# Kernel optimization log

Measured on AMD Instinct MI355X. Metric: run time of the kernel, lower is better.

Reference implementation:

```python
import jax, jax.numpy as jnp
import numpy as np


def setup_inputs() -> dict:
    key = jax.random.key(0)
    k1, k2 = jax.random.split(key)
    B, N, M, D = 4, 8192, 8192, 3
    input1 = jax.random.normal(k1, (B, N, D), dtype=jnp.float32)
    input2 = jax.random.normal(k2, (B, M, D), dtype=jnp.float32)
    return {"input1": input1, "input2": input2}


def reference(input1, input2):
    x2 = jnp.sum(input1 * input1, axis=-1)              # [B, N]
    y2 = jnp.sum(input2 * input2, axis=-1)              # [B, M]
    xy = jnp.einsum('bnd,bmd->bnm', input1, input2)     # [B, N, M]
    d2 = x2[:, :, None] + y2[:, None, :] - 2.0 * xy     # [B, N, M]
    d2 = jnp.maximum(d2, 0.0)
    dist1 = jnp.min(d2, axis=2)  # [B, N] nearest in input2 for each point in input1
    dist2 = jnp.min(d2, axis=1)  # [B, M] nearest in input1 for each point in input2
    # Chamfer loss: mean of both directional terms
    return jnp.mean(dist1) + jnp.mean(dist2)
```

## Files before the change

kernel.cpp:

```cpp
#include <hip/hip_runtime.h>

#define NB    4
#define NPTS  8192
#define QPB   64
#define WPB   8

typedef float v2f __attribute__((ext_vector_type(2)));

struct TPair { v2f xx, yy, zz, ww; };

__global__ void pack_pts(const float* __restrict__ a, const float* __restrict__ b,
                         float4* __restrict__ q4a, float4* __restrict__ q4b,
                         TPair* __restrict__ tpa, TPair* __restrict__ tpb) {
    const int npair = NB * NPTS / 2;
    int i = blockIdx.x * blockDim.x + threadIdx.x;
    const float* src = a;
    float4* q4 = q4a;  TPair* tp = tpa;
    int p = i;
    if (i >= npair) { src = b; q4 = q4b; tp = tpb; p = i - npair; }

    float x0 = src[6*p+0], y0 = src[6*p+1], z0 = src[6*p+2];
    float x1 = src[6*p+3], y1 = src[6*p+4], z1 = src[6*p+5];
    float w0 = 0.5f * (x0*x0 + y0*y0 + z0*z0);
    float w1 = 0.5f * (x1*x1 + y1*y1 + z1*z1);
    q4[2*p]   = make_float4(x0, y0, z0, w0);
    q4[2*p+1] = make_float4(x1, y1, z1, w1);
    TPair t;
    t.xx = (v2f){x0, x1}; t.yy = (v2f){y0, y1};
    t.zz = (v2f){z0, z1}; t.ww = (v2f){w0, w1};
    tp[p] = t;
}

#define GROUP(XX, YY, ZZ, WW, ACC) do {                                        \
    v2f r_;                                                                    \
    asm("v_pk_mul_f32 %0, %1, %2"     : "=v"(r_) : "v"(nqx), "s"(XX));         \
    asm("v_pk_fma_f32 %0, %1, %2, %0" : "+v"(r_) : "v"(nqy), "s"(YY));         \
    asm("v_pk_fma_f32 %0, %1, %2, %0" : "+v"(r_) : "v"(nqz), "s"(ZZ));         \
    asm("v_pk_add_f32 %0, %0, %1"     : "+v"(r_) : "s"(WW));                   \
    asm("v_min3_f32 %0, %0, %1, %2"   : "+v"(ACC) : "v"(r_.x), "v"(r_.y));     \
} while (0)

__launch_bounds__(512, 8)
__global__ void chamfer_min(const float4* __restrict__ q4a, const float4* __restrict__ q4b,
                            const TPair* __restrict__ tpa, const TPair* __restrict__ tpb,
                            float* __restrict__ accum) {
    __shared__ float red[512];

    const int dir = blockIdx.y;
    const int bb  = blockIdx.x / (NPTS / QPB);
    const int blk = blockIdx.x % (NPTS / QPB);

    const float4* __restrict__ Q = (dir == 0 ? q4a : q4b) + bb * NPTS;
    const TPair*  __restrict__ T = (dir == 0 ? tpb : tpa) + bb * (NPTS / 2);

    const int lane = threadIdx.x & 63;
    const int wave = __builtin_amdgcn_readfirstlane((int)(threadIdx.x >> 6));

    const float4 q = Q[blk * QPB + lane];
    v2f nqx = (v2f){-q.x, -q.x};
    v2f nqy = (v2f){-q.y, -q.y};
    v2f nqz = (v2f){-q.z, -q.z};

    const int PPW = NPTS / 2 / WPB;
    const TPair* __restrict__ Tw = T + wave * PPW;

    float acc0 = 1e30f, acc1 = 1e30f, acc2 = 1e30f, acc3 = 1e30f;

    for (int p = 0; p < PPW; p += 4) {
        TPair t0 = Tw[p + 0];
        TPair t1 = Tw[p + 1];
        TPair t2 = Tw[p + 2];
        TPair t3 = Tw[p + 3];
        GROUP(t0.xx, t0.yy, t0.zz, t0.ww, acc0);
        GROUP(t1.xx, t1.yy, t1.zz, t1.ww, acc1);
        GROUP(t2.xx, t2.yy, t2.zz, t2.ww, acc2);
        GROUP(t3.xx, t3.yy, t3.zz, t3.ww, acc3);
    }
    float acc = fminf(fminf(acc0, acc1), fminf(acc2, acc3));

    red[threadIdx.x] = acc;
    __syncthreads();

    if (threadIdx.x < 64) {
        float v = red[lane];
#pragma unroll
        for (int w = 1; w < WPB; ++w) v = fminf(v, red[lane + 64 * w]);
        float dist = fmaxf(2.0f * (q.w + v), 0.0f);
        for (int off = 32; off > 0; off >>= 1)
            dist += __shfl_xor(dist, off, 64);
        if (lane == 0) atomicAdd(&accum[dir], dist);
    }
}

__global__ void finish(const float* __restrict__ accum, float* __restrict__ out) {
    out[0] = (accum[0] + accum[1]) * (1.0f / (NB * NPTS));
}

extern "C" void kernel_launch(void* const* d_in, const int* in_sizes, int n_in,
                              void* d_out, int out_size, void* d_ws, size_t ws_size,
                              hipStream_t stream) {
    const float* in1 = (const float*)d_in[0];
    const float* in2 = (const float*)d_in[1];

    const int tot   = NB * NPTS;
    const int npair = tot / 2;

    char* ws = (char*)d_ws;
    float*  accum = (float*)ws;
    float4* q4a   = (float4*)(ws + 256);
    float4* q4b   = q4a + tot;
    TPair*  tpa   = (TPair*)(q4b + tot);
    TPair*  tpb   = tpa + npair;

    hipMemsetAsync(accum, 0, 2 * sizeof(float), stream);

    pack_pts<<<dim3((2 * npair) / 256), 256, 0, stream>>>(in1, in2, q4a, q4b, tpa, tpb);

    dim3 grid(NB * (NPTS / QPB), 2);
    chamfer_min<<<grid, 512, 0, stream>>>(q4a, q4b, tpa, tpb, accum);

    finish<<<1, 1, 0, stream>>>(accum, (float*)d_out);
}
```

Before: 72.88 us.

## Swap roles: hold queries in registers, stream targets per lane

The min kernel is inverted. Before, each lane held one query and targets were broadcast through scalar operands. Now each block keeps 16 queries uniformly in registers as pre-negated packed pairs and each lane streams its own target pairs with vector loads, software-prefetched one iteration ahead. Each loaded target pair is reused across 16 queries, and the per-query minimum is reduced with wave shuffles and a small shared array. The cost is higher register pressure (launch bounds lowered to 3 waves per SIMD), more blocks, and a larger packed query buffer.

New measurement: 81.48 us. 11.8% more time.

```diff
diff --git a/kernel.cpp b/kernel.cpp
--- a/kernel.cpp
+++ b/kernel.cpp
@@ -2,93 +2,121 @@
 
 #define NB    4
 #define NPTS  8192
-#define QPB   64
-#define WPB   8
+#define QPB2  16
+#define TPB   256
+#define ITERS (NPTS / 2 / TPB)
 
 typedef float v2f __attribute__((ext_vector_type(2)));
+typedef float v4f __attribute__((ext_vector_type(4)));
 
 struct TPair { v2f xx, yy, zz, ww; };
 
 __global__ void pack_pts(const float* __restrict__ a, const float* __restrict__ b,
-                         float4* __restrict__ q4a, float4* __restrict__ q4b,
-                         TPair* __restrict__ tpa, TPair* __restrict__ tpb) {
+                         TPair* __restrict__ tpa, TPair* __restrict__ tpb,
+                         float* __restrict__ nqa, float* __restrict__ nqb) {
     const int npair = NB * NPTS / 2;
     int i = blockIdx.x * blockDim.x + threadIdx.x;
-    const float* src = a;
-    float4* q4 = q4a;  TPair* tp = tpa;
+    const float* src = a;  TPair* tp = tpa;  float* nq = nqa;
     int p = i;
-    if (i >= npair) { src = b; q4 = q4b; tp = tpb; p = i - npair; }
+    if (i >= npair) { src = b; tp = tpb; nq = nqb; p = i - npair; }
 
     float x0 = src[6*p+0], y0 = src[6*p+1], z0 = src[6*p+2];
     float x1 = src[6*p+3], y1 = src[6*p+4], z1 = src[6*p+5];
     float w0 = 0.5f * (x0*x0 + y0*y0 + z0*z0);
     float w1 = 0.5f * (x1*x1 + y1*y1 + z1*z1);
-    q4[2*p]   = make_float4(x0, y0, z0, w0);
-    q4[2*p+1] = make_float4(x1, y1, z1, w1);
+
     TPair t;
     t.xx = (v2f){x0, x1}; t.yy = (v2f){y0, y1};
     t.zz = (v2f){z0, z1}; t.ww = (v2f){w0, w1};
     tp[p] = t;
+
+    v4f* o = (v4f*)(nq + (size_t)2 * p * 8);
+    o[0] = (v4f){-x0, -x0, -y0, -y0};
+    o[1] = (v4f){-z0, -z0,  w0, 0.f};
+    o[2] = (v4f){-x1, -x1, -y1, -y1};
+    o[3] = (v4f){-z1, -z1,  w1, 0.f};
 }
 
-#define GROUP(XX, YY, ZZ, WW, ACC) do {                                        \
-    v2f r_;                                                                    \
-    asm("v_pk_mul_f32 %0, %1, %2"     : "=v"(r_) : "v"(nqx), "s"(XX));         \
-    asm("v_pk_fma_f32 %0, %1, %2, %0" : "+v"(r_) : "v"(nqy), "s"(YY));         \
-    asm("v_pk_fma_f32 %0, %1, %2, %0" : "+v"(r_) : "v"(nqz), "s"(ZZ));         \
-    asm("v_pk_add_f32 %0, %0, %1"     : "+v"(r_) : "s"(WW));                   \
-    asm("v_min3_f32 %0, %0, %1, %2"   : "+v"(ACC) : "v"(r_.x), "v"(r_.y));     \
+#define GROUPV(J) do {                                                          \
+    v2f r_;                                                                     \
+    asm("v_pk_mul_f32 %0, %1, %2"     : "=v"(r_) : "v"(qn[3*(J)+0]), "v"(xx_)); \
+    asm("v_pk_fma_f32 %0, %1, %2, %0" : "+v"(r_) : "v"(qn[3*(J)+1]), "v"(yy_)); \
+    asm("v_pk_fma_f32 %0, %1, %2, %0" : "+v"(r_) : "v"(qn[3*(J)+2]), "v"(zz_)); \
+    asm("v_pk_add_f32 %0, %0, %1"     : "+v"(r_) : "v"(ww_));                   \
+    asm("v_min3_f32 %0, %0, %1, %2"   : "+v"(acc[J]) : "v"(r_.x), "v"(r_.y));   \
 } while (0)
 
-__launch_bounds__(512, 8)
-__global__ void chamfer_min(const float4* __restrict__ q4a, const float4* __restrict__ q4b,
-                            const TPair* __restrict__ tpa, const TPair* __restrict__ tpb,
+__launch_bounds__(TPB, 3)
+__global__ void chamfer_min(const TPair* __restrict__ tpa, const TPair* __restrict__ tpb,
+                            const float* __restrict__ nqa, const float* __restrict__ nqb,
                             float* __restrict__ accum) {
-    __shared__ float red[512];
+    __shared__ float red[4][QPB2];
 
-    const int dir = blockIdx.y;
-    const int bb  = blockIdx.x / (NPTS / QPB);
-    const int blk = blockIdx.x % (NPTS / QPB);
+    const int qblk = blockIdx.x;
+    const int bb   = blockIdx.y;
+    const int dir  = blockIdx.z;
 
-    const float4* __restrict__ Q = (dir == 0 ? q4a : q4b) + bb * NPTS;
-    const TPair*  __restrict__ T = (dir == 0 ? tpb : tpa) + bb * (NPTS / 2);
+    const TPair* __restrict__ T  = (dir == 0 ? tpb : tpa) + bb * (NPTS / 2);
+    const float* __restrict__ NQ = (dir == 0 ? nqa : nqb) + ((size_t)bb * NPTS + qblk * QPB2) * 8;
+
+    v2f qn[3 * QPB2];
+#pragma unroll
+    for (int i = 0; i < 3 * QPB2; ++i) {
+        int q = i / 3, c = i % 3;
+        qn[i] = *(const v2f*)(NQ + q * 8 + c * 2);
+    }
+
+    float acc[QPB2];
+#pragma unroll
+    for (int j = 0; j < QPB2; ++j) acc[j] = 1e30f;
+
+    const v4f* __restrict__ T4 = (const v4f*)T;
+    const int i0 = threadIdx.x;
+    v4f tl = T4[2 * i0], th = T4[2 * i0 + 1];
+
+#pragma unroll 1
+    for (int it = 0; it < ITERS; ++it) {
+        int ni = (i0 + (it + 1) * TPB) & (NPTS / 2 - 1);
+        v4f ntl = T4[2 * ni], nth = T4[2 * ni + 1];
+
+        v2f xx_ = __builtin_shufflevector(tl, tl, 0, 1);
+        v2f yy_ = __builtin_shufflevector(tl, tl, 2, 3);
+        v2f zz_ = __builtin_shufflevector(th, th, 0, 1);
+        v2f ww_ = __builtin_shufflevector(th, th, 2, 3);
+#pragma unroll
+        for (int j = 0; j < QPB2; ++j) GROUPV(j);
+
+        tl = ntl; th = nth;
+    }
+
+#pragma unroll
+    for (int j = 0; j < QPB2; ++j) {
+        acc[j] = fminf(acc[j], __shfl_xor(acc[j], 32));
+        acc[j] = fminf(acc[j], __shfl_xor(acc[j], 16));
+        acc[j] = fminf(acc[j], __shfl_xor(acc[j], 8));
+        acc[j] = fminf(acc[j], __shfl_xor(acc[j], 4));
+        acc[j] = fminf(acc[j], __shfl_xor(acc[j], 2));
+        acc[j] = fminf(acc[j], __shfl_xor(acc[j], 1));
+    }
 
     const int lane = threadIdx.x & 63;
-    const int wave = __builtin_amdgcn_readfirstlane((int)(threadIdx.x >> 6));
-
-    const float4 q = Q[blk * QPB + lane];
-    v2f nqx = (v2f){-q.x, -q.x};
-    v2f nqy = (v2f){-q.y, -q.y};
-    v2f nqz = (v2f){-q.z, -q.z};
-
-    const int PPW = NPTS / 2 / WPB;
-    const TPair* __restrict__ Tw = T + wave * PPW;
-
-    float acc0 = 1e30f, acc1 = 1e30f, acc2 = 1e30f, acc3 = 1e30f;
-
-    for (int p = 0; p < PPW; p += 4) {
-        TPair t0 = Tw[p + 0];
-        TPair t1 = Tw[p + 1];
-        TPair t2 = Tw[p + 2];
-        TPair t3 = Tw[p + 3];
-        GROUP(t0.xx, t0.yy, t0.zz, t0.ww, acc0);
-        GROUP(t1.xx, t1.yy, t1.zz, t1.ww, acc1);
-        GROUP(t2.xx, t2.yy, t2.zz, t2.ww, acc2);
-        GROUP(t3.xx, t3.yy, t3.zz, t3.ww, acc3);
+    const int wave = threadIdx.x >> 6;
+    if (lane == 0) {
+#pragma unroll
+        for (int j = 0; j < QPB2; ++j) red[wave][j] = acc[j];
     }
-    float acc = fminf(fminf(acc0, acc1), fminf(acc2, acc3));
-
-    red[threadIdx.x] = acc;
     __syncthreads();
 
-    if (threadIdx.x < 64) {
-        float v = red[lane];
-#pragma unroll
-        for (int w = 1; w < WPB; ++w) v = fminf(v, red[lane + 64 * w]);
-        float dist = fmaxf(2.0f * (q.w + v), 0.0f);
-        for (int off = 32; off > 0; off >>= 1)
-            dist += __shfl_xor(dist, off, 64);
-        if (lane == 0) atomicAdd(&accum[dir], dist);
+    if (threadIdx.x < QPB2) {
+        const int j = threadIdx.x;
+        float v = fminf(fminf(red[0][j], red[1][j]), fminf(red[2][j], red[3][j]));
+        float q2h = NQ[j * 8 + 6];
+        float dist = fmaxf(2.0f * (q2h + v), 0.0f);
+        dist += __shfl_xor(dist, 8, 16);
+        dist += __shfl_xor(dist, 4, 16);
+        dist += __shfl_xor(dist, 2, 16);
+        dist += __shfl_xor(dist, 1, 16);
+        if (j == 0) atomicAdd(&accum[dir], dist);
     }
 }
 
@@ -107,17 +135,17 @@
 
     char* ws = (char*)d_ws;
     float*  accum = (float*)ws;
-    float4* q4a   = (float4*)(ws + 256);
-    float4* q4b   = q4a + tot;
-    TPair*  tpa   = (TPair*)(q4b + tot);
+    TPair*  tpa   = (TPair*)(ws + 256);
     TPair*  tpb   = tpa + npair;
+    float*  nqa   = (float*)(tpb + npair);
+    float*  nqb   = nqa + (size_t)tot * 8;
 
     hipMemsetAsync(accum, 0, 2 * sizeof(float), stream);
 
-    pack_pts<<<dim3((2 * npair) / 256), 256, 0, stream>>>(in1, in2, q4a, q4b, tpa, tpb);
+    pack_pts<<<dim3((2 * npair) / 256), 256, 0, stream>>>(in1, in2, tpa, tpb, nqa, nqb);
 
-    dim3 grid(NB * (NPTS / QPB), 2);
-    chamfer_min<<<grid, 512, 0, stream>>>(q4a, q4b, tpa, tpb, accum);
+    dim3 grid(NPTS / QPB2, NB, 2);
+    chamfer_min<<<grid, TPB, 0, stream>>>(tpa, tpb, nqa, nqb, accum);
 
     finish<<<1, 1, 0, stream>>>(accum, (float*)d_out);
 }
```
